# Optimization experiments

Hardware: AMD Instinct MI355X
Metric: run time of the kernel (lower is better)

## Reference

```python
import jax, jax.numpy as jnp
import numpy as np

SIGMA = 1.0  # kernel bandwidth (init kwarg)

VS = 4096   # src vertices
VT = 4096   # tar vertices
FS = 8192   # src triangles
FT = 8192   # tar triangles
FR = 8192   # reference triangles


def setup_inputs() -> dict:
    key = jax.random.key(0)
    k0, k1, k2, k3, k4, k5 = jax.random.split(key, 6)
    src_vertices = jax.random.normal(k0, (VS, 3), dtype=jnp.float32)
    src_indices = jax.random.randint(k1, (FS, 3), 0, VS, dtype=jnp.int64)
    tar_vertices = jax.random.normal(k2, (VT, 3), dtype=jnp.float32)
    tar_indices = jax.random.randint(k3, (FT, 3), 0, VT, dtype=jnp.int64)
    ref_normals = 0.1 * jax.random.normal(k4, (FR, 3), dtype=jnp.float32)
    ref_centers = jax.random.normal(k5, (FR, 3), dtype=jnp.float32)
    return {
        "src_vertices": src_vertices,
        "src_indices": src_indices,
        "tar_vertices": tar_vertices,
        "tar_indices": tar_indices,
        "ref_normals": ref_normals,
        "ref_centers": ref_centers,
    }


def _tri_normals_centers(vertices, indices):
    tris = vertices[indices]               # [F, 3, 3]
    a, b, c = tris[:, 0, :], tris[:, 1, :], tris[:, 2, :]
    normals = 0.5 * jnp.cross(a - b, c - b)  # [F, 3]
    centers = tris.sum(axis=1) / 3.0         # [F, 3]
    return normals, centers


def _sqdist(src, tar):
    # d[i, j] = ||tar_i - src_j||^2  -> shape [Nt, Ns]
    s2 = jnp.sum(src * src, axis=-1)  # [Ns]
    t2 = jnp.sum(tar * tar, axis=-1)  # [Nt]
    return t2[:, None] + s2[None, :] - 2.0 * (tar @ src.T)


def _cauchy(d):
    return 1.0 / (1.0 + d / SIGMA) ** 2


def _energy(sn, sc, tn, tc):
    e1 = jnp.sum((sn @ sn.T) * _cauchy(_sqdist(sc, sc)))
    e2 = jnp.sum((tn @ sn.T) * _cauchy(_sqdist(sc, tc)))
    e3 = jnp.sum((tn @ tn.T) * _cauchy(_sqdist(tc, tc)))
    return e1 - 2.0 * e2 + e3


def reference(src_vertices, src_indices, tar_vertices, tar_indices, ref_normals, ref_centers):
    src_n, src_c = _tri_normals_centers(src_vertices, src_indices)
    tar_n, tar_c = _tri_normals_centers(tar_vertices, tar_indices)
    energy = _energy(src_n, src_c, ref_normals, ref_centers)
    energy = energy + _energy(tar_n, tar_c, ref_normals, ref_centers)
    energy = energy + 0.8 * _energy(src_n, src_c, tar_n, tar_c)
    return energy
```

## Files before the change

kernel.cpp:

```cpp
#include <hip/hip_runtime.h>

#define NSEG 8192
#define NPTS (3 * NSEG)
#define NSUP 96
#define NXB  96
#define NYG  25

typedef short bf16x8 __attribute__((ext_vector_type(8)));
typedef float f32x16 __attribute__((ext_vector_type(16)));
typedef unsigned short u16;

__device__ __forceinline__ u16 f2bf(float x) {
    unsigned u = __builtin_bit_cast(unsigned, x);
    return (u16)((u + 0x7FFFu + ((u >> 16) & 1u)) >> 16);
}
__device__ __forceinline__ float bf2f(u16 h) {
    unsigned u = ((unsigned)h) << 16;
    return __builtin_bit_cast(float, u);
}

__device__ __forceinline__ void compute_point(
    int seg, int f,
    const float* __restrict__ sv, const int* __restrict__ si,
    const float* __restrict__ tv, const int* __restrict__ ti,
    const float* __restrict__ rn, const float* __restrict__ rc,
    float& cx, float& cy, float& cz, float& nx, float& ny, float& nz)
{
    if (seg == 2) {
        nx = rn[3*f];   ny = rn[3*f+1]; nz = rn[3*f+2];
        cx = rc[3*f];   cy = rc[3*f+1]; cz = rc[3*f+2];
    } else {
        const float* v  = (seg == 0) ? sv : tv;
        const int*   nd = (seg == 0) ? si : ti;
        int i0 = nd[3*f], i1 = nd[3*f+1], i2 = nd[3*f+2];
        float ax = v[3*i0], ay = v[3*i0+1], az = v[3*i0+2];
        float bx = v[3*i1], by = v[3*i1+1], bz = v[3*i1+2];
        float gx = v[3*i2], gy = v[3*i2+1], gz = v[3*i2+2];
        float ux = ax-bx, uy = ay-by, uz = az-bz;
        float wx = gx-bx, wy = gy-by, wz = gz-bz;
        nx = 0.5f*(uy*wz - uz*wy);
        ny = 0.5f*(uz*wx - ux*wz);
        nz = 0.5f*(ux*wy - uy*wx);
        cx = (ax+bx+gx)*(1.0f/3.0f);
        cy = (ay+by+gy)*(1.0f/3.0f);
        cz = (az+bz+gz)*(1.0f/3.0f);
    }
}

__global__ void setup_feats(const float* __restrict__ sv, const int* __restrict__ si,
                            const float* __restrict__ tv, const int* __restrict__ ti,
                            const float* __restrict__ rn, const float* __restrict__ rc,
                            u16* __restrict__ ws, float* __restrict__ out) {
    int p = blockIdx.x * 256 + threadIdx.x;
    if (p == 0) out[0] = 0.0f;
    if (p >= NPTS) return;
    int seg = p >> 13, f = p & (NSEG - 1);
    float cx, cy, cz, nx, ny, nz;
    compute_point(seg, f, sv, si, tv, ti, rn, rc, cx, cy, cz, nx, ny, nz);

    const u16 ONE = 0x3F80;
    float s = cx*cx + cy*cy + cz*cz;
    u16 chx = f2bf(cx), chy = f2bf(cy), chz = f2bf(cz);
    u16 clx = f2bf(cx - bf2f(chx)), cly = f2bf(cy - bf2f(chy)), clz = f2bf(cz - bf2f(chz));
    u16 sh  = f2bf(s);
    u16 sl  = f2bf(s - bf2f(sh));
    u16 m2hx = f2bf(-2.0f*bf2f(chx)), m2hy = f2bf(-2.0f*bf2f(chy)), m2hz = f2bf(-2.0f*bf2f(chz));
    u16 m2lx = f2bf(-2.0f*bf2f(clx)), m2ly = f2bf(-2.0f*bf2f(cly)), m2lz = f2bf(-2.0f*bf2f(clz));
    u16 nhx = f2bf(nx), nhy = f2bf(ny), nhz = f2bf(nz);
    u16 nlx = f2bf(nx - bf2f(nhx)), nly = f2bf(ny - bf2f(nhy)), nlz = f2bf(nz - bf2f(nhz));

    u16 at[16] = {chx,chy,chz, clx,cly,clz, chx,chy,chz, sh, sl, ONE, ONE, ONE, 0, 0};
    u16 bt[16] = {m2hx,m2hy,m2hz, m2hx,m2hy,m2hz, m2lx,m2ly,m2lz, ONE, ONE, sh, sl, ONE, 0, 0};
    u16 an[16] = {nhx,nhy,nhz, nlx,nly,nlz, nhx,nhy,nhz, 0,0,0,0,0,0,0};
    u16 bn[16] = {nhx,nhy,nhz, nhx,nhy,nhz, nlx,nly,nlz, 0,0,0,0,0,0,0};

    bf16x8* A8 = (bf16x8*)ws;
    bf16x8* B8 = A8 + (size_t)NPTS*4;
    bf16x8 v0, v1, v2, v3;
    #pragma unroll
    for (int k = 0; k < 8; ++k) { v0[k] = (short)at[k]; v1[k] = (short)at[k+8];
                                  v2[k] = (short)an[k]; v3[k] = (short)an[k+8]; }
    A8[(size_t)p*4+0] = v0; A8[(size_t)p*4+1] = v1; A8[(size_t)p*4+2] = v2; A8[(size_t)p*4+3] = v3;
    #pragma unroll
    for (int k = 0; k < 8; ++k) { v0[k] = (short)bt[k]; v1[k] = (short)bt[k+8];
                                  v2[k] = (short)bn[k]; v3[k] = (short)bn[k+8]; }
    B8[(size_t)p*4+0] = v0; B8[(size_t)p*4+1] = v1; B8[(size_t)p*4+2] = v2; B8[(size_t)p*4+3] = v3;
}

__launch_bounds__(256, 2)
__global__ void energy_mfma(const u16* __restrict__ ws, float* __restrict__ out) {
    const int tid  = threadIdx.x;
    const int lane = tid & 63, wid = tid >> 6;
    const int half = lane >> 5, r32 = lane & 31;

    const int X  = blockIdx.x;
    const int g  = blockIdx.y;
    const int y0  = (g < 24) ? 2*g : 48;
    const int ycnt = (g < 24) ? 2 : 1;
    const int gi = X >> 5;

    const bf16x8* A8 = (const bf16x8*)ws;
    const bf16x8* B8 = A8 + (size_t)NPTS*4;

    const int pi = X*256 + wid*32 + r32;
    const bf16x8 at0 = A8[pi*4 + half];
    const bf16x8 an0 = A8[pi*4 + 2 + half];
    const bf16x8 at1 = A8[pi*4 + 512 + half];
    const bf16x8 an1 = A8[pi*4 + 514 + half];

    f32x16 Z;
    #pragma unroll
    for (int k = 0; k < 16; ++k) Z[k] = 0.0f;

    const int lofs = r32*4 + half;

    auto yinfo = [&](int y, int& vo, float& w) {
        int J = X + y; if (J >= NSUP) J -= NSUP;
        int jg = J >> 5;
        float base_w;
        if (gi == jg)                 base_w = (gi == 2) ? 2.0f : 1.8f;
        else if (gi == 2 || jg == 2)  base_w = -1.0f;
        else                          base_w = -0.8f;
        const float mult = (y == 0 || y == 48) ? 1.0f : 2.0f;
        w = base_w * mult;
        vo = J*1024 + lofs;
    };

#define EPI(CT, CN, TS0, TS1) do {                                            \
        _Pragma("unroll")                                                     \
        for (int gq = 0; gq < 4; ++gq) {                                      \
            float t0 = CT[4*gq+0], t1 = CT[4*gq+1];                           \
            float t2 = CT[4*gq+2], t3 = CT[4*gq+3];                           \
            float q0 = t0*t0, q1 = t1*t1, q2 = t2*t2, q3 = t3*t3;             \
            float s01 = q0*q1, s23 = q2*q3;                                   \
            float r   = __builtin_amdgcn_rcpf(s01*s23);                       \
            float u   = __builtin_fmaf(CN[4*gq+1], q0, CN[4*gq+0]*q1);        \
            float v   = __builtin_fmaf(CN[4*gq+3], q2, CN[4*gq+2]*q3);        \
            float num = __builtin_fmaf(v, s01, u*s23);                        \
            if (gq & 1) TS1 = __builtin_fmaf(num, r, TS1);                    \
            else        TS0 = __builtin_fmaf(num, r, TS0);                    \
        }                                                                     \
    } while (0)

    float acc = 0.0f;
    int vo; float w;
    yinfo(y0, vo, w);

    bf16x8 bt0 = B8[vo],       bn0 = B8[vo + 2];
    bf16x8 bt1 = B8[vo + 128], bn1 = B8[vo + 130];

    #pragma unroll 1
    for (int yy = 0; yy < ycnt; ++yy) {
        int von; float wn;
        yinfo((yy + 1 < ycnt) ? (y0 + yy + 1) : (y0 + yy), von, wn);

        float tsA0 = 0.0f, tsA1 = 0.0f;
        float tsB0 = 0.0f, tsB1 = 0.0f;
        #pragma unroll 2
        for (int jt = 0; jt < 8; ++jt) {
            const int pofs = (jt < 6) ? (vo + (jt + 2)*128) : (von + (jt - 6)*128);
            bf16x8 pt = B8[pofs];
            bf16x8 pn = B8[pofs + 2];

            f32x16 ct, cn;
            ct = __builtin_amdgcn_mfma_f32_32x32x16_bf16(at0, bt0, Z, 0, 0, 0);
            cn = __builtin_amdgcn_mfma_f32_32x32x16_bf16(an0, bn0, Z, 0, 0, 0);
            EPI(ct, cn, tsA0, tsA1);
            ct = __builtin_amdgcn_mfma_f32_32x32x16_bf16(at1, bt0, Z, 0, 0, 0);
            cn = __builtin_amdgcn_mfma_f32_32x32x16_bf16(an1, bn0, Z, 0, 0, 0);
            EPI(ct, cn, tsB0, tsB1);

            bt0 = bt1; bn0 = bn1;
            bt1 = pt;  bn1 = pn;
        }
        acc = __builtin_fmaf(w, tsA0 + tsA1, acc);
        acc = __builtin_fmaf(w, tsB0 + tsB1, acc);
        vo = von; w = wn;
    }
#undef EPI

    for (int off = 32; off; off >>= 1) acc += __shfl_down(acc, off, 64);
    __shared__ float partial[4];
    if ((tid & 63) == 0) partial[wid] = acc;
    __syncthreads();
    if (tid == 0)
        atomicAdd(out, (partial[0] + partial[1]) + (partial[2] + partial[3]));
}

extern "C" void kernel_launch(void* const* d_in, const int* in_sizes, int n_in,
                              void* d_out, int out_size, void* d_ws, size_t ws_size,
                              hipStream_t stream) {
    const float* sv = (const float*)d_in[0];
    const int*   si = (const int*)d_in[1];
    const float* tv = (const float*)d_in[2];
    const int*   ti = (const int*)d_in[3];
    const float* rn = (const float*)d_in[4];
    const float* rc = (const float*)d_in[5];
    float* out = (float*)d_out;
    u16*   ws  = (u16*)d_ws;

    setup_feats<<<NPTS/256, 256, 0, stream>>>(sv, si, tv, ti, rn, rc, ws, out);
    dim3 grid(NXB, NYG);
    energy_mfma<<<grid, 256, 0, stream>>>(ws, out);
}
```

Measured before the change: 112.3 us.

## Pack epilogue math into float2 vectors and drop manual B-operand prefetch pipeline

Rewrites the Cauchy epilogue to use two-wide float vectors, so the compiler can emit packed FP32 multiplies (v_pk_mul_f32) for the squares and cross products. It also removes the hand-written two-deep software prefetch of B fragments across y iterations. Loads are now issued directly inside a loop unrolled by 4, leaving latency hiding to the compiler. This cuts VALU instruction count in the epilogue-bound loop, but risks exposing global load latency that the old rotation hid.

```diff
diff --git a/kernel.cpp b/kernel.cpp
--- a/kernel.cpp
+++ b/kernel.cpp
@@ -8,6 +8,7 @@
 
 typedef short bf16x8 __attribute__((ext_vector_type(8)));
 typedef float f32x16 __attribute__((ext_vector_type(16)));
+typedef float f32x2  __attribute__((ext_vector_type(2)));
 typedef unsigned short u16;
 
 __device__ __forceinline__ u16 f2bf(float x) {
@@ -129,13 +130,17 @@
 #define EPI(CT, CN, TS0, TS1) do {                                            \
         _Pragma("unroll")                                                     \
         for (int gq = 0; gq < 4; ++gq) {                                      \
-            float t0 = CT[4*gq+0], t1 = CT[4*gq+1];                           \
-            float t2 = CT[4*gq+2], t3 = CT[4*gq+3];                           \
-            float q0 = t0*t0, q1 = t1*t1, q2 = t2*t2, q3 = t3*t3;             \
-            float s01 = q0*q1, s23 = q2*q3;                                   \
+            f32x2 t01 = {CT[4*gq+0], CT[4*gq+1]};                             \
+            f32x2 t23 = {CT[4*gq+2], CT[4*gq+3]};                             \
+            f32x2 cA  = {CN[4*gq+0], CN[4*gq+1]};                             \
+            f32x2 cB  = {CN[4*gq+2], CN[4*gq+3]};                             \
+            f32x2 qA = t01*t01, qB = t23*t23;            \
+            float s01 = qA[0]*qA[1], s23 = qB[0]*qB[1];                       \
             float r   = __builtin_amdgcn_rcpf(s01*s23);                       \
-            float u   = __builtin_fmaf(CN[4*gq+1], q0, CN[4*gq+0]*q1);        \
-            float v   = __builtin_fmaf(CN[4*gq+3], q2, CN[4*gq+2]*q3);        \
+            f32x2 sqA = {qA[1], qA[0]}, sqB = {qB[1], qB[0]};                 \
+            f32x2 pA = cA*sqA, pB = cB*sqB;              \
+            float u = pA[0] + pA[1];                                          \
+            float v = pB[0] + pB[1];                                          \
             float num = __builtin_fmaf(v, s01, u*s23);                        \
             if (gq & 1) TS1 = __builtin_fmaf(num, r, TS1);                    \
             else        TS0 = __builtin_fmaf(num, r, TS0);                    \
@@ -143,39 +148,28 @@
     } while (0)
 
     float acc = 0.0f;
-    int vo; float w;
-    yinfo(y0, vo, w);
-
-    bf16x8 bt0 = B8[vo],       bn0 = B8[vo + 2];
-    bf16x8 bt1 = B8[vo + 128], bn1 = B8[vo + 130];
-
     #pragma unroll 1
     for (int yy = 0; yy < ycnt; ++yy) {
-        int von; float wn;
-        yinfo((yy + 1 < ycnt) ? (y0 + yy + 1) : (y0 + yy), von, wn);
+        int vo; float w;
+        yinfo(y0 + yy, vo, w);
 
         float tsA0 = 0.0f, tsA1 = 0.0f;
         float tsB0 = 0.0f, tsB1 = 0.0f;
-        #pragma unroll 2
+        #pragma unroll 4
         for (int jt = 0; jt < 8; ++jt) {
-            const int pofs = (jt < 6) ? (vo + (jt + 2)*128) : (von + (jt - 6)*128);
-            bf16x8 pt = B8[pofs];
-            bf16x8 pn = B8[pofs + 2];
+            bf16x8 bt = B8[vo + jt*128];
+            bf16x8 bn = B8[vo + jt*128 + 2];
 
             f32x16 ct, cn;
-            ct = __builtin_amdgcn_mfma_f32_32x32x16_bf16(at0, bt0, Z, 0, 0, 0);
-            cn = __builtin_amdgcn_mfma_f32_32x32x16_bf16(an0, bn0, Z, 0, 0, 0);
+            ct = __builtin_amdgcn_mfma_f32_32x32x16_bf16(at0, bt, Z, 0, 0, 0);
+            cn = __builtin_amdgcn_mfma_f32_32x32x16_bf16(an0, bn, Z, 0, 0, 0);
             EPI(ct, cn, tsA0, tsA1);
-            ct = __builtin_amdgcn_mfma_f32_32x32x16_bf16(at1, bt0, Z, 0, 0, 0);
-            cn = __builtin_amdgcn_mfma_f32_32x32x16_bf16(an1, bn0, Z, 0, 0, 0);
+            ct = __builtin_amdgcn_mfma_f32_32x32x16_bf16(at1, bt, Z, 0, 0, 0);
+            cn = __builtin_amdgcn_mfma_f32_32x32x16_bf16(an1, bn, Z, 0, 0, 0);
             EPI(ct, cn, tsB0, tsB1);
-
-            bt0 = bt1; bn0 = bn1;
-            bt1 = pt;  bn1 = pn;
         }
         acc = __builtin_fmaf(w, tsA0 + tsA1, acc);
         acc = __builtin_fmaf(w, tsB0 + tsB1, acc);
-        vo = von; w = wn;
     }
 #undef EPI
 
```

Measured after the change: 115.9 us. +3.2%, slower.
